# Performance work log

Measured on AMD Instinct MI355X. Metric: run time of the kernel, lower is better.

## Reference

```python
import jax, jax.numpy as jnp
import numpy as np

EPS = 1e-5

def ln(x, w, b):
    mu = jnp.mean(x, axis=-1, keepdims=True)
    var = jnp.mean(jnp.square(x - mu), axis=-1, keepdims=True)
    return (x - mu) * jax.lax.rsqrt(var + EPS) * w + b

def setup_inputs() -> dict:
    key = jax.random.key(0)
    ks = jax.random.split(key, 4)
    B, H, W, C = 8, 224, 224, 96
    Cout = 2 * C  # 192
    x = jax.random.normal(ks[0], (B, H, W, C), dtype=jnp.float32)
    saliency_map = jax.random.uniform(ks[1], (B, H, W), dtype=jnp.float32)
    # PatchMerging reduction: Linear(4C -> 2C, bias=False), xavier_uniform init
    limit = float(np.sqrt(6.0 / (4 * C + Cout)))
    merge_w = jax.random.uniform(ks[2], (Cout, 4 * C), minval=-limit, maxval=limit, dtype=jnp.float32)
    return {
        "x": x,
        "saliency_map": saliency_map,
        "merge_w": merge_w,
        "merge_norm_w": jnp.ones((4 * C,), jnp.float32),
        "merge_norm_b": jnp.zeros((4 * C,), jnp.float32),
        "vss_norm_w": jnp.ones((Cout,), jnp.float32),
        "vss_norm_b": jnp.zeros((Cout,), jnp.float32),
        "asram_norm_w": jnp.ones((Cout,), jnp.float32),
        "asram_norm_b": jnp.zeros((Cout,), jnp.float32),
        "final_norm_w": jnp.ones((Cout,), jnp.float32),
        "final_norm_b": jnp.zeros((Cout,), jnp.float32),
    }

def reference(x, saliency_map, merge_w, merge_norm_w, merge_norm_b,
              vss_norm_w, vss_norm_b, asram_norm_w, asram_norm_b,
              final_norm_w, final_norm_b):
    # --- PatchMerging: [B,H,W,C] -> [B,H/2,W/2,2C] ---
    x0 = x[:, 0::2, 0::2, :]
    x1 = x[:, 1::2, 0::2, :]
    x2 = x[:, 0::2, 1::2, :]
    x3 = x[:, 1::2, 1::2, :]
    xm = jnp.concatenate([x0, x1, x2, x3], axis=-1)          # [B,H/2,W/2,4C]
    xm = ln(xm, merge_norm_w, merge_norm_b)
    xs = jnp.einsum('bhwi,oi->bhwo', xm, merge_w)            # [B,H/2,W/2,2C]
    # saliency adaptation (bilinear resize, align_corners=False); mock ASRAM ignores it
    B, Hn, Wn, _ = xs.shape
    _sal = jax.image.resize(saliency_map[:, None], (B, 1, Hn, Wn), method='bilinear')
    del _sal  # unused by mock ASRAM, kept for fidelity of the dataflow
    # --- Mock DualVSSBlock: x + LayerNorm(x) ---
    xv = xs + ln(xs, vss_norm_w, vss_norm_b)
    # --- Mock ASRAM: LayerNorm over channels (permute round-trip is a no-op here) ---
    xa = ln(xv, asram_norm_w, asram_norm_b)
    # --- Final LayerNorm ---
    return ln(xa, final_norm_w, final_norm_b)
```

## Files before the change

kernel.cpp:

```cpp
#include <hip/hip_runtime.h>
#include <hip/hip_bf16.h>
#include <cstdint>
#include <cstddef>

typedef float f32x4  __attribute__((ext_vector_type(4)));
typedef short bf16x8 __attribute__((ext_vector_type(8)));
typedef int   i32x4  __attribute__((ext_vector_type(4)));

#define LN_EPS 1e-5f

static __device__ __forceinline__ unsigned short f2bf(float f) {
    __hip_bfloat16 h = __float2bfloat16(f);
    union { __hip_bfloat16 b; unsigned short u; } cv; cv.b = h;
    return cv.u;
}
static __device__ __forceinline__ float bf2f(unsigned short h) {
    return __uint_as_float(((unsigned int)h) << 16);
}

__global__ void prep_w_kernel(const float* __restrict__ W,
                              const float* __restrict__ g,
                              unsigned short* __restrict__ wsh) {
    int o = blockIdx.x * 256 + threadIdx.x;
    if (o >= 192 * 384) return;
    int j    = o & 7;
    int lane = (o >> 3) & 63;
    int t    = o >> 9;
    int nf   = t % 12;
    int kk   = t / 12;
    int n = nf * 16 + (lane & 15);
    int k = kk * 32 + (lane >> 4) * 8 + j;
    wsh[o] = f2bf(g[k] * W[n * 384 + k]);
}

__global__ void prep_sc_kernel(const float* __restrict__ W,
                               const float* __restrict__ g,
                               const float* __restrict__ b,
                               float* __restrict__ s2,
                               float* __restrict__ c0) {
    int o = threadIdx.x;
    if (o >= 192) return;
    const float* wr = W + o * 384;
    float a = 0.f, c = 0.f;
    for (int i = 0; i < 384; i++) { float w = wr[i]; a += g[i] * w; c += b[i] * w; }
    s2[o] = a; c0[o] = c;
}

template <bool USE_WS>
__global__ __launch_bounds__(256, 3)
void fused_kernel(const float* __restrict__ x,
                  const unsigned short* __restrict__ wsh,
                  const float* __restrict__ s2p, const float* __restrict__ c0p,
                  const float* __restrict__ Wf,
                  const float* __restrict__ mw, const float* __restrict__ mb,
                  const float* __restrict__ vw, const float* __restrict__ vb,
                  const float* __restrict__ aw, const float* __restrict__ ab,
                  const float* __restrict__ fw, const float* __restrict__ fb,
                  float* __restrict__ out) {
    __shared__ __align__(16) unsigned char lds[49152];

    const int tid = threadIdx.x;
    const int r   = tid >> 3;
    const int u   = tid & 7;
    const int q   = u >> 1;
    const int hh  = u & 1;

    const int wv = tid >> 6;
    const int l  = tid & 63;
    const int g  = l >> 4;
    const int cl = l & 15;

    float mu = 0.f, rs = 0.f;

    {
        const int R   = blockIdx.x * 32 + r;
        const int b   = R / 12544;
        const int rem = R - b * 12544;
        const int h2  = rem / 112;
        const int w2  = rem - h2 * 112;
        const int h   = 2 * h2 + (q & 1);
        const int w   = 2 * w2 + (q >> 1);
        const f32x4* src = (const f32x4*)(x + (((size_t)b * 224 + h) * 224 + w) * 96 + hh * 48);
        f32x4 v[12];
        #pragma unroll
        for (int i = 0; i < 12; i++) v[i] = src[i];

        if (USE_WS) {
            #pragma unroll
            for (int p = 0; p < 6; p++) {
                union { unsigned short u16[8]; i32x4 v4; } ph, pl;
                #pragma unroll
                for (int half = 0; half < 2; half++) {
                    const int i = 2 * p + half;
                    #pragma unroll
                    for (int e = 0; e < 4; e++) {
                        float a = v[i][e];
                        unsigned short hi = f2bf(a);
                        ph.u16[4 * half + e] = hi;
                        pl.u16[4 * half + e] = f2bf(a - bf2f(hi));
                    }
                }
                const int slot = 6 * u + p;
                const int boff = (slot * 16) ^ ((r & 7) << 4);
                *(i32x4*)(&lds[r * 768 + boff])         = ph.v4;
                *(i32x4*)(&lds[24576 + r * 768 + boff]) = pl.v4;
            }
            float s = 0.f;
            #pragma unroll
            for (int i = 0; i < 12; i++) {
                #pragma unroll
                for (int e = 0; e < 4; e++) s += v[i][e];
            }
            s += __shfl_xor(s, 1); s += __shfl_xor(s, 2); s += __shfl_xor(s, 4);
            mu = s * (1.f / 384.f);
            float sd = 0.f;
            #pragma unroll
            for (int i = 0; i < 12; i++) {
                #pragma unroll
                for (int e = 0; e < 4; e++) { float d = v[i][e] - mu; sd += d * d; }
            }
            sd += __shfl_xor(sd, 1); sd += __shfl_xor(sd, 2); sd += __shfl_xor(sd, 4);
            rs = rsqrtf(sd * (1.f / 384.f) + LN_EPS);
        } else {
            float s = 0.f;
            #pragma unroll
            for (int i = 0; i < 12; i++) {
                #pragma unroll
                for (int e = 0; e < 4; e++) s += v[i][e];
            }
            s += __shfl_xor(s, 1); s += __shfl_xor(s, 2); s += __shfl_xor(s, 4);
            mu = s * (1.f / 384.f);
            float sd = 0.f;
            #pragma unroll
            for (int i = 0; i < 12; i++) {
                #pragma unroll
                for (int e = 0; e < 4; e++) { float d = v[i][e] - mu; sd += d * d; }
            }
            sd += __shfl_xor(sd, 1); sd += __shfl_xor(sd, 2); sd += __shfl_xor(sd, 4);
            rs = rsqrtf(sd * (1.f / 384.f) + LN_EPS);

            const f32x4* mwv = (const f32x4*)(mw + q * 96 + hh * 48);
            const f32x4* mbv = (const f32x4*)(mb + q * 96 + hh * 48);
            #pragma unroll
            for (int p = 0; p < 6; p++) {
                union { unsigned short u16[8]; i32x4 v4; } ph, pl;
                #pragma unroll
                for (int half = 0; half < 2; half++) {
                    const int i = 2 * p + half;
                    f32x4 w4 = mwv[i], b4 = mbv[i];
                    #pragma unroll
                    for (int e = 0; e < 4; e++) {
                        float a = (v[i][e] - mu) * rs * w4[e] + b4[e];
                        unsigned short hi = f2bf(a);
                        ph.u16[4 * half + e] = hi;
                        pl.u16[4 * half + e] = f2bf(a - bf2f(hi));
                    }
                }
                const int slot = 6 * u + p;
                const int boff = (slot * 16) ^ ((r & 7) << 4);
                *(i32x4*)(&lds[r * 768 + boff])         = ph.v4;
                *(i32x4*)(&lds[24576 + r * 768 + boff]) = pl.v4;
            }
        }
    }
    __syncthreads();

    f32x4 acc[2][3];
    #pragma unroll
    for (int mf = 0; mf < 2; mf++)
        #pragma unroll
        for (int t = 0; t < 3; t++) acc[mf][t] = (f32x4){0.f, 0.f, 0.f, 0.f};

    if (USE_WS) {
        #pragma unroll
        for (int half = 0; half < 2; half++) {
            bf16x8 B[6][3];
            #pragma unroll
            for (int kx = 0; kx < 6; kx++) {
                const int kk = 6 * half + kx;
                const bf16x8* bp = (const bf16x8*)wsh + ((kk * 12 + 3 * wv) * 64 + l);
                B[kx][0] = bp[0]; B[kx][1] = bp[64]; B[kx][2] = bp[128];
            }
            #pragma unroll
            for (int kx = 0; kx < 6; kx++) {
                asm volatile("" : "+v"(B[kx][0]), "+v"(B[kx][1]), "+v"(B[kx][2]));
            }
            #pragma unroll
            for (int kx = 0; kx < 6; kx++) {
                const int kk = 6 * half + kx;
                #pragma unroll
                for (int mf = 0; mf < 2; mf++) {
                    const int row  = 16 * mf + cl;
                    const int boff = (kk * 64 + g * 16) ^ ((row & 7) << 4);
                    bf16x8 afh = *(const bf16x8*)(&lds[row * 768 + boff]);
                    bf16x8 afl = *(const bf16x8*)(&lds[24576 + row * 768 + boff]);
                    #pragma unroll
                    for (int t = 0; t < 3; t++) {
                        acc[mf][t] = __builtin_amdgcn_mfma_f32_16x16x32_bf16(afh, B[kx][t], acc[mf][t], 0, 0, 0);
                        acc[mf][t] = __builtin_amdgcn_mfma_f32_16x16x32_bf16(afl, B[kx][t], acc[mf][t], 0, 0, 0);
                    }
                }
            }
        }
    } else {
        #pragma unroll
        for (int kk = 0; kk < 12; kk++) {
            bf16x8 bh[3];
            #pragma unroll
            for (int t = 0; t < 3; t++) {
                const int n = (3 * wv + t) * 16 + cl;
                const float* wp = Wf + n * 384 + kk * 32 + g * 8;
                f32x4 lo = *(const f32x4*)wp;
                f32x4 hi4 = *(const f32x4*)(wp + 4);
                bf16x8 hbb;
                #pragma unroll
                for (int e = 0; e < 4; e++) {
                    hbb[e] = (short)f2bf(lo[e]); hbb[4 + e] = (short)f2bf(hi4[e]);
                }
                bh[t] = hbb;
            }
            #pragma unroll
            for (int mf = 0; mf < 2; mf++) {
                const int row  = 16 * mf + cl;
                const int boff = (kk * 64 + g * 16) ^ ((row & 7) << 4);
                bf16x8 afh = *(const bf16x8*)(&lds[row * 768 + boff]);
                bf16x8 afl = *(const bf16x8*)(&lds[24576 + row * 768 + boff]);
                #pragma unroll
                for (int t = 0; t < 3; t++) {
                    acc[mf][t] = __builtin_amdgcn_mfma_f32_16x16x32_bf16(afh, bh[t], acc[mf][t], 0, 0, 0);
                    acc[mf][t] = __builtin_amdgcn_mfma_f32_16x16x32_bf16(afl, bh[t], acc[mf][t], 0, 0, 0);
                }
            }
        }
    }
    __syncthreads();

    {
        float* xsl = (float*)lds;
        #pragma unroll
        for (int mf = 0; mf < 2; mf++)
            #pragma unroll
            for (int t = 0; t < 3; t++) {
                const int col = 48 * wv + 16 * t + cl;
                #pragma unroll
                for (int rg = 0; rg < 4; rg++) {
                    const int row = 16 * mf + 4 * g + rg;
                    xsl[row * 196 + col] = acc[mf][t][rg];
                }
            }
    }
    __syncthreads();

    {
        const float* rowp = (const float*)lds + r * 196 + u * 24;
        float vv[24];
        #pragma unroll
        for (int i = 0; i < 6; i++) {
            f32x4 t4 = *(const f32x4*)(rowp + 4 * i);
            #pragma unroll
            for (int e = 0; e < 4; e++) vv[4 * i + e] = t4[e];
        }
        if (USE_WS) {
            const f32x4* s2v = (const f32x4*)(s2p + u * 24);
            const f32x4* c0v = (const f32x4*)(c0p + u * 24);
            #pragma unroll
            for (int i = 0; i < 6; i++) {
                f32x4 sv = s2v[i], cv = c0v[i];
                #pragma unroll
                for (int e = 0; e < 4; e++)
                    vv[4 * i + e] = rs * (vv[4 * i + e] - mu * sv[e]) + cv[e];
            }
        }
        float s1 = 0.f;
        #pragma unroll
        for (int i = 0; i < 24; i++) s1 += vv[i];
        s1 += __shfl_xor(s1, 1); s1 += __shfl_xor(s1, 2); s1 += __shfl_xor(s1, 4);
        const float mu1 = s1 * (1.f / 192.f);
        float d1 = 0.f;
        #pragma unroll
        for (int i = 0; i < 24; i++) { float d = vv[i] - mu1; d1 += d * d; }
        d1 += __shfl_xor(d1, 1); d1 += __shfl_xor(d1, 2); d1 += __shfl_xor(d1, 4);
        const float r1 = rsqrtf(d1 * (1.f / 192.f) + LN_EPS);

        const f32x4* vwv = (const f32x4*)(vw + u * 24);
        const f32x4* vbv = (const f32x4*)(vb + u * 24);
        float s2s = 0.f;
        #pragma unroll
        for (int i = 0; i < 6; i++) {
            f32x4 w4 = vwv[i], b4 = vbv[i];
            #pragma unroll
            for (int e = 0; e < 4; e++) {
                float xs0 = vv[4 * i + e];
                float xv0 = xs0 + (xs0 - mu1) * r1 * w4[e] + b4[e];
                vv[4 * i + e] = xv0;
                s2s += xv0;
            }
        }
        s2s += __shfl_xor(s2s, 1); s2s += __shfl_xor(s2s, 2); s2s += __shfl_xor(s2s, 4);
        const float mu2 = s2s * (1.f / 192.f);
        float d2 = 0.f;
        #pragma unroll
        for (int i = 0; i < 24; i++) { float d = vv[i] - mu2; d2 += d * d; }
        d2 += __shfl_xor(d2, 1); d2 += __shfl_xor(d2, 2); d2 += __shfl_xor(d2, 4);
        const float r2 = rsqrtf(d2 * (1.f / 192.f) + LN_EPS);

        const f32x4* awv = (const f32x4*)(aw + u * 24);
        const f32x4* abv = (const f32x4*)(ab + u * 24);
        float s3 = 0.f;
        #pragma unroll
        for (int i = 0; i < 6; i++) {
            f32x4 w4 = awv[i], b4 = abv[i];
            #pragma unroll
            for (int e = 0; e < 4; e++) {
                float xa0 = (vv[4 * i + e] - mu2) * r2 * w4[e] + b4[e];
                vv[4 * i + e] = xa0;
                s3 += xa0;
            }
        }
        s3 += __shfl_xor(s3, 1); s3 += __shfl_xor(s3, 2); s3 += __shfl_xor(s3, 4);
        const float mu3 = s3 * (1.f / 192.f);
        float d3 = 0.f;
        #pragma unroll
        for (int i = 0; i < 24; i++) { float d = vv[i] - mu3; d3 += d * d; }
        d3 += __shfl_xor(d3, 1); d3 += __shfl_xor(d3, 2); d3 += __shfl_xor(d3, 4);
        const float r3 = rsqrtf(d3 * (1.f / 192.f) + LN_EPS);

        const f32x4* fwv = (const f32x4*)(fw + u * 24);
        const f32x4* fbv = (const f32x4*)(fb + u * 24);
        float* op = out + (size_t)(blockIdx.x * 32 + r) * 192 + u * 24;
        #pragma unroll
        for (int i = 0; i < 6; i++) {
            f32x4 w4 = fwv[i], b4 = fbv[i];
            f32x4 o4;
            #pragma unroll
            for (int e = 0; e < 4; e++)
                o4[e] = (vv[4 * i + e] - mu3) * r3 * w4[e] + b4[e];
            *(f32x4*)(op + 4 * i) = o4;
        }
    }
}

extern "C" void kernel_launch(void* const* d_in, const int* in_sizes, int n_in,
                              void* d_out, int out_size, void* d_ws, size_t ws_size,
                              hipStream_t stream) {
    const float* x  = (const float*)d_in[0];
    const float* W  = (const float*)d_in[2];
    const float* mw = (const float*)d_in[3];
    const float* mb = (const float*)d_in[4];
    const float* vw = (const float*)d_in[5];
    const float* vb = (const float*)d_in[6];
    const float* aw = (const float*)d_in[7];
    const float* ab = (const float*)d_in[8];
    const float* fw = (const float*)d_in[9];
    const float* fb = (const float*)d_in[10];
    float* out = (float*)d_out;

    const int rows   = 8 * 112 * 112;
    const int blocks = rows / 32;

    unsigned short* wsh = (unsigned short*)d_ws;
    float* s2 = (float*)((char*)d_ws + 192 * 384 * 2);
    float* c0 = s2 + 192;

    if (ws_size >= (size_t)(192 * 384 * 2 + 2 * 192 * 4)) {
        prep_w_kernel<<<288, 256, 0, stream>>>(W, mw, wsh);
        prep_sc_kernel<<<1, 192, 0, stream>>>(W, mw, mb, s2, c0);
        fused_kernel<true><<<blocks, 256, 0, stream>>>(x, wsh, s2, c0, W, mw, mb,
                                                       vw, vb, aw, ab, fw, fb, out);
    } else {
        fused_kernel<false><<<blocks, 256, 0, stream>>>(x, wsh, s2, c0, W, mw, mb,
                                                        vw, vb, aw, ab, fw, fb, out);
    }
}
```

Before: 90.65 us.

## Pipeline weight loads with triple-buffered inline asm and parallelize scale prep

Replaces the two-half bulk register load of bf16 weight fragments with a three-deep rotating buffer. Raw global_load_dwordx4 instructions and explicit vmcnt waits keep two k-steps of weight loads in flight while MFMAs consume the current one. This cuts register pressure and hides global latency. Separately, the per-output scale and offset prep kernel now uses one 64-lane wavefront per output with a shuffle reduction, instead of a single 192-thread block looping serially. Inline asm with manual waitcnt is fragile: the compiler does not track these loads, so correctness relies on the hand-counted vmcnt values.

```diff
diff --git a/kernel.cpp b/kernel.cpp
--- a/kernel.cpp
+++ b/kernel.cpp
@@ -38,12 +38,19 @@
                                const float* __restrict__ b,
                                float* __restrict__ s2,
                                float* __restrict__ c0) {
-    int o = threadIdx.x;
-    if (o >= 192) return;
+    const int o = blockIdx.x;
+    const int j = threadIdx.x;
     const float* wr = W + o * 384;
     float a = 0.f, c = 0.f;
-    for (int i = 0; i < 384; i++) { float w = wr[i]; a += g[i] * w; c += b[i] * w; }
-    s2[o] = a; c0[o] = c;
+    #pragma unroll
+    for (int i = 0; i < 6; i++) {
+        const int k = j + 64 * i;
+        float w = wr[k];
+        a += g[k] * w; c += b[k] * w;
+    }
+    #pragma unroll
+    for (int d = 1; d < 64; d <<= 1) { a += __shfl_xor(a, d); c += __shfl_xor(c, d); }
+    if (j == 0) { s2[o] = a; c0[o] = c; }
 }
 
 template <bool USE_WS>
@@ -172,36 +179,53 @@
         for (int t = 0; t < 3; t++) acc[mf][t] = (f32x4){0.f, 0.f, 0.f, 0.f};
 
     if (USE_WS) {
-        #pragma unroll
-        for (int half = 0; half < 2; half++) {
-            bf16x8 B[6][3];
-            #pragma unroll
-            for (int kx = 0; kx < 6; kx++) {
-                const int kk = 6 * half + kx;
-                const bf16x8* bp = (const bf16x8*)wsh + ((kk * 12 + 3 * wv) * 64 + l);
-                B[kx][0] = bp[0]; B[kx][1] = bp[64]; B[kx][2] = bp[128];
-            }
-            #pragma unroll
-            for (int kx = 0; kx < 6; kx++) {
-                asm volatile("" : "+v"(B[kx][0]), "+v"(B[kx][1]), "+v"(B[kx][2]));
-            }
-            #pragma unroll
-            for (int kx = 0; kx < 6; kx++) {
-                const int kk = 6 * half + kx;
-                #pragma unroll
-                for (int mf = 0; mf < 2; mf++) {
-                    const int row  = 16 * mf + cl;
-                    const int boff = (kk * 64 + g * 16) ^ ((row & 7) << 4);
-                    bf16x8 afh = *(const bf16x8*)(&lds[row * 768 + boff]);
-                    bf16x8 afl = *(const bf16x8*)(&lds[24576 + row * 768 + boff]);
-                    #pragma unroll
-                    for (int t = 0; t < 3; t++) {
-                        acc[mf][t] = __builtin_amdgcn_mfma_f32_16x16x32_bf16(afh, B[kx][t], acc[mf][t], 0, 0, 0);
-                        acc[mf][t] = __builtin_amdgcn_mfma_f32_16x16x32_bf16(afl, B[kx][t], acc[mf][t], 0, 0, 0);
-                    }
-                }
-            }
-        }
+        bf16x8 B0[3], B1[3], B2[3];
+
+        auto issue = [&](int KK, bf16x8* Bb) {
+            const bf16x8* bp = (const bf16x8*)wsh + ((KK * 12 + 3 * wv) * 64 + l);
+            asm volatile("global_load_dwordx4 %0, %1, off" : "=v"(Bb[0]) : "v"(bp));
+            asm volatile("global_load_dwordx4 %0, %1, off" : "=v"(Bb[1]) : "v"(bp + 64));
+            asm volatile("global_load_dwordx4 %0, %1, off" : "=v"(Bb[2]) : "v"(bp + 128));
+        };
+        auto consume = [&](int KK, const bf16x8* Bb) {
+            #pragma unroll
+            for (int mf = 0; mf < 2; mf++) {
+                const int row  = 16 * mf + cl;
+                const int boff = (KK * 64 + g * 16) ^ ((row & 7) << 4);
+                bf16x8 afh = *(const bf16x8*)(&lds[row * 768 + boff]);
+                bf16x8 afl = *(const bf16x8*)(&lds[24576 + row * 768 + boff]);
+                #pragma unroll
+                for (int t = 0; t < 3; t++) {
+                    acc[mf][t] = __builtin_amdgcn_mfma_f32_16x16x32_bf16(afh, Bb[t], acc[mf][t], 0, 0, 0);
+                    acc[mf][t] = __builtin_amdgcn_mfma_f32_16x16x32_bf16(afl, Bb[t], acc[mf][t], 0, 0, 0);
+                }
+            }
+        };
+
+        issue(0, B0); issue(1, B1);
+
+        #define STEP(KK, BUF, NXTBUF, VM)                                   \
+            do {                                                            \
+                if ((KK) + 2 < 12) issue((KK) + 2, NXTBUF);                 \
+                asm volatile("s_waitcnt vmcnt(" #VM ")" ::: "memory");      \
+                __builtin_amdgcn_sched_barrier(0);                          \
+                consume((KK), BUF);                                         \
+            } while (0)
+
+        STEP(0,  B0, B2, 6);
+        STEP(1,  B1, B0, 6);
+        STEP(2,  B2, B1, 6);
+        STEP(3,  B0, B2, 6);
+        STEP(4,  B1, B0, 6);
+        STEP(5,  B2, B1, 6);
+        STEP(6,  B0, B2, 6);
+        STEP(7,  B1, B0, 6);
+        STEP(8,  B2, B1, 6);
+        STEP(9,  B0, B2, 6);
+        STEP(10, B1, B0, 3);
+        STEP(11, B2, B1, 0);
+        #undef STEP
+        __builtin_amdgcn_sched_barrier(0);
     } else {
         #pragma unroll
         for (int kk = 0; kk < 12; kk++) {
@@ -364,7 +388,7 @@
 
     if (ws_size >= (size_t)(192 * 384 * 2 + 2 * 192 * 4)) {
         prep_w_kernel<<<288, 256, 0, stream>>>(W, mw, wsh);
-        prep_sc_kernel<<<1, 192, 0, stream>>>(W, mw, mb, s2, c0);
+        prep_sc_kernel<<<192, 64, 0, stream>>>(W, mw, mb, s2, c0);
         fused_kernel<true><<<blocks, 256, 0, stream>>>(x, wsh, s2, c0, W, mw, mb,
                                                        vw, vb, aw, ab, fw, fb, out);
     } else {
```

New measurement: 80.26 us. -11.5%, faster.
